# Optimization experiments

Measured on AMD Instinct MI355X. Metric: run time of the kernel, lower is better.

The kernel has to match this reference:

```python
import jax, jax.numpy as jnp
import numpy as np

TEMPERATURE = 0.5
EPS_NORM = 1e-12   # F.normalize eps
EPS_DEN = 1e-8     # denominator clamp


def setup_inputs() -> dict:
    key = jax.random.key(0)
    k1, k2 = jax.random.split(key)
    B, D = 4096, 256
    return {
        "proj_feat1": jax.random.normal(k1, (B, D), dtype=jnp.float32),
        "proj_feat2": jax.random.normal(k2, (B, D), dtype=jnp.float32),
    }


def _l2_normalize(x):
    n = jnp.sqrt(jnp.sum(x * x, axis=1, keepdims=True))
    return x / jnp.maximum(n, EPS_NORM)


def reference(proj_feat1, proj_feat2):
    B = proj_feat1.shape[0]
    z1 = _l2_normalize(proj_feat1)
    z2 = _l2_normalize(proj_feat2)
    z = jnp.concatenate([z1, z2], axis=0)          # [2B, D], unit rows
    # cosine similarity of unit-norm rows == plain matmul (GEMM instead of
    # the O(N^2*D) broadcasted intermediate in the torch source)
    sim = jnp.matmul(z, z.T)                        # [2B, 2B]
    s = jnp.exp(sim / TEMPERATURE)                  # [2B, 2B]
    idx = jnp.arange(2 * B)
    pos_idx = (idx + B) % (2 * B)                   # roll(eye, B, dim=1) positions
    numerator = s[idx, pos_idx]                     # [2B]
    # negatives: everything except the diagonal
    diag = jnp.diagonal(s)
    denominator = jnp.sum(s, axis=1) - diag         # sum * (1 - eye)
    denominator = jnp.maximum(denominator, EPS_DEN)
    loss = jnp.mean(-jnp.log(numerator / denominator))
    return loss
```

## Files before the change

### kernel.cpp

```cpp
#include <hip/hip_runtime.h>
#include <hip/hip_bf16.h>

#define NTOT 8192
#define BB   4096
#define DD   256
#define NWAVES 2048
#define NBLK (NWAVES / 4)
#define NCHUNK 33024

typedef __attribute__((ext_vector_type(8))) short short8v;
typedef __attribute__((ext_vector_type(4))) float f32x4;

__device__ __forceinline__ unsigned short f2bf(float f) {
    union { __hip_bfloat16 h; unsigned short u; } cv;
    cv.h = __float2bfloat16(f);
    return cv.u;
}

__global__ __launch_bounds__(256) void k_normalize(
    const float* __restrict__ x1, const float* __restrict__ x2,
    unsigned short* __restrict__ zbf,
    float* __restrict__ selfdot, float* __restrict__ posdot,
    float* __restrict__ S, float* __restrict__ out)
{
    if (blockIdx.x < 8) {
        float4 z4 = make_float4(0.f, 0.f, 0.f, 0.f);
        *(float4*)(S + blockIdx.x * 1024 + threadIdx.x * 4) = z4;
        if (blockIdx.x == 0 && threadIdx.x == 0) out[0] = 0.0f;
    }

    const int lane = threadIdx.x & 63;
    const int pair = blockIdx.x * 4 + (threadIdx.x >> 6);

    const float4 a = *(const float4*)(x1 + (size_t)pair * DD + lane * 4);
    const float4 b = *(const float4*)(x2 + (size_t)pair * DD + lane * 4);

    float s1 = a.x * a.x + a.y * a.y + a.z * a.z + a.w * a.w;
    float s2 = b.x * b.x + b.y * b.y + b.z * b.z + b.w * b.w;
#pragma unroll
    for (int off = 1; off < 64; off <<= 1) {
        s1 += __shfl_xor(s1, off);
        s2 += __shfl_xor(s2, off);
    }
    const float inv1 = 1.0f / fmaxf(sqrtf(s1), 1e-12f);
    const float inv2 = 1.0f / fmaxf(sqrtf(s2), 1e-12f);

    const float4 z1 = make_float4(a.x * inv1, a.y * inv1, a.z * inv1, a.w * inv1);
    const float4 z2 = make_float4(b.x * inv2, b.y * inv2, b.z * inv2, b.w * inv2);

    float sd1 = z1.x * z1.x + z1.y * z1.y + z1.z * z1.z + z1.w * z1.w;
    float sd2 = z2.x * z2.x + z2.y * z2.y + z2.z * z2.z + z2.w * z2.w;
    float pd  = z1.x * z2.x + z1.y * z2.y + z1.z * z2.z + z1.w * z2.w;
#pragma unroll
    for (int off = 1; off < 64; off <<= 1) {
        sd1 += __shfl_xor(sd1, off);
        sd2 += __shfl_xor(sd2, off);
        pd  += __shfl_xor(pd, off);
    }

    ushort4 u1, u2;
    u1.x = f2bf(z1.x); u1.y = f2bf(z1.y); u1.z = f2bf(z1.z); u1.w = f2bf(z1.w);
    u2.x = f2bf(z2.x); u2.y = f2bf(z2.y); u2.z = f2bf(z2.z); u2.w = f2bf(z2.w);
    *(ushort4*)(zbf + (size_t)pair * DD + lane * 4) = u1;
    *(ushort4*)(zbf + (size_t)(pair + BB) * DD + lane * 4) = u2;

    if (lane == 0) {
        selfdot[pair] = sd1;
        selfdot[pair + BB] = sd2;
        posdot[pair] = pd;
        posdot[pair + BB] = pd;
    }
}

__global__ __launch_bounds__(256, 2) void k_simsum(
    const unsigned short* __restrict__ zbf, float* __restrict__ S)
{
    __shared__ char Bsh[4][2][8192];

    const int tid  = threadIdx.x;
    const int lane = tid & 63;
    const int wv   = tid >> 6;
    const int frow = lane & 15;
    const int g    = lane >> 4;
    const int v    = blockIdx.x * 4 + wv;

    const int sBeg = (129 * v) >> 3;
    const int sEnd = (129 * (v + 1)) >> 3;

    int r = 0, C = 0;
    while (C + 512 - 4 * r <= sBeg) { C += 512 - 4 * r; ++r; }
    int t = sBeg - C;

    int srcOff[8];
#pragma unroll
    for (int ri = 0; ri < 8; ++ri) {
        const int lc = ri * 2 + (lane >> 5);
        srcOff[ri] = lc * 512 + (((lane & 31) ^ (lc & 7)) << 4);
    }

    const int base0 = frow * 512 + g * 16;
    const int bmask = (frow & 7) << 4;
    int addrs[8];
#pragma unroll
    for (int kk = 0; kk < 8; ++kk) addrs[kk] = (base0 + kk * 64) ^ bmask;

    char* buf0 = &Bsh[wv][0][0];
    char* buf1 = &Bsh[wv][1][0];

#define STAGE(r_, t_, bufp)                                                        \
    do {                                                                           \
        const char* gs_ = (const char*)zbf + (size_t)(r_) * 32768                  \
                          + (size_t)(t_) * 8192;                                   \
        _Pragma("unroll")                                                          \
        for (int ri_ = 0; ri_ < 8; ++ri_)                                          \
            __builtin_amdgcn_global_load_lds(                                      \
                (const __attribute__((address_space(1))) unsigned int*)(gs_ + srcOff[ri_]), \
                (__attribute__((address_space(3))) unsigned int*)((bufp) + ri_ * 1024 + lane * 16), \
                16, 0, 0);                                                         \
    } while (0)

#define ADV(rr, tt)                                                                \
    do { if (++(tt) >= 512 - 4 * (rr)) { ++(rr); (tt) = 0; } } while (0)

    short8v Afrag[4][8];
#pragma unroll
    for (int rt = 0; rt < 4; ++rt) {
        const unsigned short* ap =
            zbf + (size_t)(64 * r + rt * 16 + frow) * DD + g * 8;
#pragma unroll
        for (int kk = 0; kk < 8; ++kk)
            Afrag[rt][kk] = *(const short8v*)(ap + kk * 32);
    }

    float rs[4][4];
#pragma unroll
    for (int rt = 0; rt < 4; ++rt)
#pragma unroll
        for (int q = 0; q < 4; ++q) rs[rt][q] = 0.0f;

    STAGE(r, t, buf0);
    int pr = r, pt = t;
    ADV(pr, pt);
    STAGE(pr, pt, buf1);
    ADV(pr, pt);

    int cur = 0;
    int cr = r, ct = t;
    for (int s = sBeg; s < sEnd; ++s) {
        if (s + 1 < sEnd) {
            asm volatile("s_waitcnt vmcnt(8)" ::: "memory");
        } else {
            asm volatile("s_waitcnt vmcnt(0)" ::: "memory");
        }
        __builtin_amdgcn_sched_barrier(0);

        char* buf = cur ? buf1 : buf0;

        f32x4 acc[4];
#pragma unroll
        for (int rt = 0; rt < 4; ++rt) {
            acc[rt][0] = 0.0f; acc[rt][1] = 0.0f;
            acc[rt][2] = 0.0f; acc[rt][3] = 0.0f;
        }
#pragma unroll
        for (int kk = 0; kk < 8; ++kk) {
            const short8v bfr = *(const short8v*)(buf + addrs[kk]);
#pragma unroll
            for (int rt = 0; rt < 4; ++rt)
                acc[rt] = __builtin_amdgcn_mfma_f32_16x16x32_bf16(
                    Afrag[rt][kk], bfr, acc[rt], 0, 0, 0);
        }

        float cs = 0.0f;
#pragma unroll
        for (int rt = 0; rt < 4; ++rt)
#pragma unroll
            for (int q = 0; q < 4; ++q) {
                const float e = exp2f(acc[rt][q] * 2.8853900817779268f);
                rs[rt][q] += e;
                cs += e;
            }
        if (ct >= 4) {
            cs += __shfl_xor(cs, 16);
            cs += __shfl_xor(cs, 32);
            if (lane < 16)
                atomicAdd(&S[64 * cr + 16 * ct + frow], cs);
        }

        if (s + 2 < sEnd) { STAGE(pr, pt, buf); ADV(pr, pt); }

        if (s + 1 < sEnd) {
            int nr = cr, nt = ct + 1;
            if (nt >= 512 - 4 * cr) { nr = cr + 1; nt = 0; }
            if (nr != cr) {
#pragma unroll
                for (int rt = 0; rt < 4; ++rt)
#pragma unroll
                    for (int q = 0; q < 4; ++q) {
                        float val = rs[rt][q];
                        val += __shfl_xor(val, 1);
                        val += __shfl_xor(val, 2);
                        val += __shfl_xor(val, 4);
                        val += __shfl_xor(val, 8);
                        if (frow == 0)
                            atomicAdd(&S[64 * cr + rt * 16 + g * 4 + q], val);
                        rs[rt][q] = 0.0f;
                    }
#pragma unroll
                for (int rt = 0; rt < 4; ++rt) {
                    const unsigned short* ap =
                        zbf + (size_t)(64 * nr + rt * 16 + frow) * DD + g * 8;
#pragma unroll
                    for (int kk = 0; kk < 8; ++kk)
                        Afrag[rt][kk] = *(const short8v*)(ap + kk * 32);
                }
            }
            cr = nr; ct = nt;
        }
        cur ^= 1;
    }

#pragma unroll
    for (int rt = 0; rt < 4; ++rt)
#pragma unroll
        for (int q = 0; q < 4; ++q) {
            float val = rs[rt][q];
            val += __shfl_xor(val, 1);
            val += __shfl_xor(val, 2);
            val += __shfl_xor(val, 4);
            val += __shfl_xor(val, 8);
            if (frow == 0)
                atomicAdd(&S[64 * cr + rt * 16 + g * 4 + q], val);
        }
#undef STAGE
#undef ADV
}

__global__ __launch_bounds__(256) void k_final(
    const float* __restrict__ S, const float* __restrict__ selfdot,
    const float* __restrict__ posdot, float* __restrict__ out)
{
    __shared__ float red[4];
    const int tid = threadIdx.x;
    const int i = blockIdx.x * 256 + tid;
    const float den = fmaxf(S[i] - expf(2.0f * selfdot[i]), 1e-8f);
    float acc = logf(den) - 2.0f * posdot[i];
#pragma unroll
    for (int off = 1; off < 64; off <<= 1) acc += __shfl_xor(acc, off);
    if ((tid & 63) == 0) red[tid >> 6] = acc;
    __syncthreads();
    if (tid == 0)
        atomicAdd(out, (red[0] + red[1] + red[2] + red[3]) * (1.0f / (float)NTOT));
}

extern "C" void kernel_launch(void* const* d_in, const int* in_sizes, int n_in,
                              void* d_out, int out_size, void* d_ws, size_t ws_size,
                              hipStream_t stream) {
    const float* x1 = (const float*)d_in[0];
    const float* x2 = (const float*)d_in[1];
    float* out = (float*)d_out;

    char* ws = (char*)d_ws;
    unsigned short* zbf = (unsigned short*)ws;
    size_t off = (size_t)NTOT * DD * sizeof(unsigned short);
    float* S = (float*)(ws + off);
    off += (size_t)NTOT * sizeof(float);
    float* selfdot = (float*)(ws + off);
    off += (size_t)NTOT * sizeof(float);
    float* posdot = (float*)(ws + off);

    k_normalize<<<dim3(BB / 4), dim3(256), 0, stream>>>(x1, x2, zbf, selfdot, posdot, S, out);
    k_simsum<<<dim3(NBLK), dim3(256), 0, stream>>>(zbf, S);
    k_final<<<dim3(NTOT / 256), dim3(256), 0, stream>>>(S, selfdot, posdot, out);
}
```

Before: 104.6 us.

## Replace per-tile column atomics with colsum buffer reduced in final kernel

Each symmetric tile's column-sum partial is now written to a dedicated colsum buffer (one slot per tile step) instead of being atomically added into S. The final kernel gathers these partials per row with a closed-form tile index. The waitcnt thresholds are relaxed by one to account for the extra outstanding store, and the main loop is marked not to unroll. This removes global atomic contention from the inner loop, at the cost of an extra workspace buffer and a serial gather loop in the final kernel, which now uses 128-thread blocks.

```diff
diff --git a/kernel.cpp b/kernel.cpp
--- a/kernel.cpp
+++ b/kernel.cpp
@@ -73,7 +73,8 @@
 }
 
 __global__ __launch_bounds__(256, 2) void k_simsum(
-    const unsigned short* __restrict__ zbf, float* __restrict__ S)
+    const unsigned short* __restrict__ zbf, float* __restrict__ S,
+    float* __restrict__ colsum)
 {
     __shared__ char Bsh[4][2][8192];
 
@@ -146,11 +147,14 @@
 
     int cur = 0;
     int cr = r, ct = t;
+#pragma unroll 1
     for (int s = sBeg; s < sEnd; ++s) {
-        if (s + 1 < sEnd) {
+        if (s == sBeg) {
             asm volatile("s_waitcnt vmcnt(8)" ::: "memory");
+        } else if (s + 1 < sEnd) {
+            asm volatile("s_waitcnt vmcnt(9)" ::: "memory");
         } else {
-            asm volatile("s_waitcnt vmcnt(0)" ::: "memory");
+            asm volatile("s_waitcnt vmcnt(1)" ::: "memory");
         }
         __builtin_amdgcn_sched_barrier(0);
 
@@ -180,12 +184,10 @@
                 rs[rt][q] += e;
                 cs += e;
             }
-        if (ct >= 4) {
-            cs += __shfl_xor(cs, 16);
-            cs += __shfl_xor(cs, 32);
-            if (lane < 16)
-                atomicAdd(&S[64 * cr + 16 * ct + frow], cs);
-        }
+        cs += __shfl_xor(cs, 16);
+        cs += __shfl_xor(cs, 32);
+        if (lane < 16)
+            colsum[(size_t)s * 16 + frow] = cs;
 
         if (s + 2 < sEnd) { STAGE(pr, pt, buf); ADV(pr, pt); }
 
@@ -236,21 +238,29 @@
 #undef ADV
 }
 
-__global__ __launch_bounds__(256) void k_final(
-    const float* __restrict__ S, const float* __restrict__ selfdot,
-    const float* __restrict__ posdot, float* __restrict__ out)
+__global__ __launch_bounds__(128) void k_final(
+    const float* __restrict__ S, const float* __restrict__ colsum,
+    const float* __restrict__ selfdot, const float* __restrict__ posdot,
+    float* __restrict__ out)
 {
-    __shared__ float red[4];
+    __shared__ float red[2];
     const int tid = threadIdx.x;
-    const int i = blockIdx.x * 256 + tid;
-    const float den = fmaxf(S[i] - expf(2.0f * selfdot[i]), 1e-8f);
+    const int i = blockIdx.x * 128 + tid;
+    float s = S[i];
+    const int cc = i >> 4, fr = i & 15;
+#pragma unroll 4
+    for (int r = 0; 4 * r + 4 <= cc; ++r) {
+        const int sidx = 2 * r * (257 - r) + (cc - 4 * r);
+        s += colsum[(size_t)sidx * 16 + fr];
+    }
+    const float den = fmaxf(s - expf(2.0f * selfdot[i]), 1e-8f);
     float acc = logf(den) - 2.0f * posdot[i];
 #pragma unroll
     for (int off = 1; off < 64; off <<= 1) acc += __shfl_xor(acc, off);
     if ((tid & 63) == 0) red[tid >> 6] = acc;
     __syncthreads();
     if (tid == 0)
-        atomicAdd(out, (red[0] + red[1] + red[2] + red[3]) * (1.0f / (float)NTOT));
+        atomicAdd(out, (red[0] + red[1]) * (1.0f / (float)NTOT));
 }
 
 extern "C" void kernel_launch(void* const* d_in, const int* in_sizes, int n_in,
@@ -268,8 +278,10 @@
     float* selfdot = (float*)(ws + off);
     off += (size_t)NTOT * sizeof(float);
     float* posdot = (float*)(ws + off);
+    off += (size_t)NTOT * sizeof(float);
+    float* colsum = (float*)(ws + off);
 
     k_normalize<<<dim3(BB / 4), dim3(256), 0, stream>>>(x1, x2, zbf, selfdot, posdot, S, out);
-    k_simsum<<<dim3(NBLK), dim3(256), 0, stream>>>(zbf, S);
-    k_final<<<dim3(NTOT / 256), dim3(256), 0, stream>>>(S, selfdot, posdot, out);
-}
+    k_simsum<<<dim3(NBLK), dim3(256), 0, stream>>>(zbf, S, colsum);
+    k_final<<<dim3(NTOT / 128), dim3(128), 0, stream>>>(S, colsum, selfdot, posdot, out);
+}
```

Measured after the change: 116.7 us. 1.12x slower.
